# Performance work log

Hardware: AMD Instinct MI355X
Metric: run time of the kernel (lower is better)

Reference implementation:

```python
import jax, jax.numpy as jnp
import numpy as np

C = 1024
MID = C // 4  # 256
B, H, W = 16, 56, 56


def setup_inputs() -> dict:
    key = jax.random.key(0)
    ks = jax.random.split(key, 8)
    x = jax.random.normal(ks[0], (B, C, H, W), dtype=jnp.float32)
    gate_values = jax.random.uniform(ks[1], (B, MID), dtype=jnp.float32)
    # MoELayer conv weights: stack of out_channels 1x1 convs -> [out, in]
    W1 = jax.random.normal(ks[2], (MID, C), dtype=jnp.float32) * (1.0 / np.sqrt(C))
    b1 = jnp.zeros((MID,), dtype=jnp.float32)
    W2 = jax.random.normal(ks[3], (MID, MID), dtype=jnp.float32) * (1.0 / np.sqrt(MID))
    b2 = jnp.zeros((MID,), dtype=jnp.float32)
    W3 = jax.random.normal(ks[4], (C, MID), dtype=jnp.float32) * (1.0 / np.sqrt(MID))
    b3 = jnp.zeros((C,), dtype=jnp.float32)
    return {"x": x, "gate_values": gate_values, "W1": W1, "b1": b1,
            "W2": W2, "b2": b2, "W3": W3, "b3": b3}


def _moe_1x1(h, gate, Wc, bc):
    # Dense equivalent of the per-channel gated 1x1 conv experts:
    # out[b,o] = (conv_o(h[b]) ) * gate[b,o] if gate[b,o] > 0 else 0
    y = jnp.einsum('bchw,oc->bohw', h, Wc) + bc[None, :, None, None]
    g = jnp.where(gate > 0, gate, 0.0)  # [B, O]
    return y * g[:, :, None, None]


def reference(x, gate_values, W1, b1, W2, b2, W3, b3):
    h = jax.nn.relu(_moe_1x1(x, gate_values, W1, b1))
    h = jax.nn.relu(_moe_1x1(h, gate_values, W2, b2))
    h = jax.nn.relu(jnp.einsum('bchw,oc->bohw', h, W3) + b3[None, :, None, None])
    return h + x
```

## Files before the change

### kernel.cpp

```cpp
#include <hip/hip_runtime.h>


#define NPIX 3136
#define BATCH 16

typedef __attribute__((ext_vector_type(8))) short short8;
typedef __attribute__((ext_vector_type(4))) float v4f;

__device__ __forceinline__ unsigned short f2bf(float f) {
    union { float f; unsigned u; } v; v.f = f;
    unsigned r = v.u + 0x7fffu + ((v.u >> 16) & 1u);
    return (unsigned short)(r >> 16);
}

__device__ __forceinline__ void ld_g2l16(const unsigned short* g, unsigned short* l) {
    __builtin_amdgcn_global_load_lds(
        (const __attribute__((address_space(1))) unsigned int*)g,
        (__attribute__((address_space(3))) unsigned int*)l,
        16, 0, 0);
}

__global__ void convert_w(const float* __restrict__ W1, const float* __restrict__ W2,
                          const float* __restrict__ W3, unsigned short* __restrict__ Wb) {
    size_t e = ((size_t)blockIdx.x * 256 + threadIdx.x) * 4;
    const float* src; size_t off;
    if (e < 262144)      { src = W1; off = e; }
    else if (e < 327680) { src = W2; off = e - 262144; }
    else                 { src = W3; off = e - 327680; }
    float4 v = *reinterpret_cast<const float4*>(&src[off]);
    uint2 p;
    p.x = (unsigned)f2bf(v.x) | ((unsigned)f2bf(v.y) << 16);
    p.y = (unsigned)f2bf(v.z) | ((unsigned)f2bf(v.w) << 16);
    *reinterpret_cast<uint2*>(&Wb[e]) = p;
}

__global__ __launch_bounds__(256, 3) void moe_block(
    const float* __restrict__ x, const unsigned short* __restrict__ Wb,
    const float* __restrict__ b1, const float* __restrict__ b2,
    const float* __restrict__ b3, const float* __restrict__ gate,
    float* __restrict__ out)
{
    __shared__ __attribute__((aligned(16))) unsigned short Wsm[256 * 32];
    __shared__ __attribute__((aligned(16))) unsigned short Hsm[64 * 256];
    __shared__ __attribute__((aligned(16))) unsigned short Xsm[64 * 32];

    const unsigned short* W1b = Wb;
    const unsigned short* W2b = Wb + 262144;
    const unsigned short* W3b = Wb + 327680;

    const int b    = blockIdx.z;
    const int p0   = blockIdx.x * 64;
    const int t    = threadIdx.x;
    const int lane = t & 63;
    const int wave = t >> 6;
    const int wm   = wave * 64;
    const int l15  = lane & 15;
    const int quad = lane >> 4;

    const int srow  = t >> 2;
    const int skoff = (t & 3) * 8;

    char* hb = reinterpret_cast<char*>(Hsm);
    v4f acc[4][4];

    #pragma unroll
    for (int i = 0; i < 4; ++i)
        #pragma unroll
        for (int j = 0; j < 4; ++j) acc[i][j] = (v4f){0.f, 0.f, 0.f, 0.f};

    {
        const unsigned short* wg = W1b + srow * 1024 + skoff;
        const int cp   = t & 15;
        const int pgrp = t >> 4;
        const float* xg = x + ((size_t)(b * 1024 + 2 * cp)) * NPIX + p0 + pgrp * 4;
        unsigned* xw = reinterpret_cast<unsigned*>(&Xsm[pgrp * 128 + 2 * cp]);

        float4 a0 = *reinterpret_cast<const float4*>(xg);
        float4 a1 = *reinterpret_cast<const float4*>(xg + NPIX);

        for (int k0 = 0; k0 < 1024; k0 += 32) {
            __syncthreads();
            ld_g2l16(wg + k0,          &Wsm[t * 8]);
            ld_g2l16(wg + k0 + 65536,  &Wsm[2048 + t * 8]);
            ld_g2l16(wg + k0 + 131072, &Wsm[4096 + t * 8]);
            ld_g2l16(wg + k0 + 196608, &Wsm[6144 + t * 8]);
            unsigned u0 = (unsigned)f2bf(a0.x) | ((unsigned)f2bf(a1.x) << 16);
            unsigned u1 = (unsigned)f2bf(a0.y) | ((unsigned)f2bf(a1.y) << 16);
            unsigned u2 = (unsigned)f2bf(a0.z) | ((unsigned)f2bf(a1.z) << 16);
            unsigned u3 = (unsigned)f2bf(a0.w) | ((unsigned)f2bf(a1.w) << 16);
            xw[0] = u0; xw[16] = u1; xw[32] = u2; xw[48] = u3;
            __syncthreads();

            if (k0 + 32 < 1024) {
                const float* xp = xg + (size_t)(k0 + 32) * NPIX;
                a0 = *reinterpret_cast<const float4*>(xp);
                a1 = *reinterpret_cast<const float4*>(xp + NPIX);
            }

            short8 rf[4], cf[4];
            #pragma unroll
            for (int mt = 0; mt < 4; ++mt)
                rf[mt] = *reinterpret_cast<const short8*>(
                    &Wsm[(wm + mt * 16 + l15) * 32 + quad * 8]);
            #pragma unroll
            for (int nt = 0; nt < 4; ++nt)
                cf[nt] = *reinterpret_cast<const short8*>(
                    &Xsm[(nt * 16 + l15) * 32 + quad * 8]);
            #pragma unroll
            for (int mt = 0; mt < 4; ++mt)
                #pragma unroll
                for (int nt = 0; nt < 4; ++nt)
                    acc[mt][nt] = __builtin_amdgcn_mfma_f32_16x16x32_bf16(
                        rf[mt], cf[nt], acc[mt][nt], 0, 0, 0);
        }
    }

    #pragma unroll
    for (int mt = 0; mt < 4; ++mt) {
        const int o = wm + mt * 16 + quad * 4;
        const float4 bi = *reinterpret_cast<const float4*>(&b1[o]);
        const float4 gv = *reinterpret_cast<const float4*>(&gate[b * 256 + o]);
        const float g0 = gv.x > 0.f ? gv.x : 0.f;
        const float g1 = gv.y > 0.f ? gv.y : 0.f;
        const float g2 = gv.z > 0.f ? gv.z : 0.f;
        const float g3 = gv.w > 0.f ? gv.w : 0.f;
        #pragma unroll
        for (int nt = 0; nt < 4; ++nt) {
            const int pix = nt * 16 + l15;
            float v0 = (acc[mt][nt][0] + bi.x) * g0;
            float v1 = (acc[mt][nt][1] + bi.y) * g1;
            float v2 = (acc[mt][nt][2] + bi.z) * g2;
            float v3 = (acc[mt][nt][3] + bi.w) * g3;
            v0 = v0 > 0.f ? v0 : 0.f; v1 = v1 > 0.f ? v1 : 0.f;
            v2 = v2 > 0.f ? v2 : 0.f; v3 = v3 > 0.f ? v3 : 0.f;
            uint2 pq;
            pq.x = (unsigned)f2bf(v0) | ((unsigned)f2bf(v1) << 16);
            pq.y = (unsigned)f2bf(v2) | ((unsigned)f2bf(v3) << 16);
            const unsigned off = (unsigned)(pix * 512 + o * 2) ^ (unsigned)((pix & 7) << 4);
            *reinterpret_cast<uint2*>(hb + off) = pq;
        }
    }

    #pragma unroll
    for (int i = 0; i < 4; ++i)
        #pragma unroll
        for (int j = 0; j < 4; ++j) acc[i][j] = (v4f){0.f, 0.f, 0.f, 0.f};

    {
        const unsigned short* wg = W2b + srow * 256 + skoff;
        for (int k0 = 0; k0 < 256; k0 += 32) {
            __syncthreads();
            ld_g2l16(wg + k0,         &Wsm[t * 8]);
            ld_g2l16(wg + k0 + 16384, &Wsm[2048 + t * 8]);
            ld_g2l16(wg + k0 + 32768, &Wsm[4096 + t * 8]);
            ld_g2l16(wg + k0 + 49152, &Wsm[6144 + t * 8]);
            __syncthreads();

            short8 rf[4], cf[4];
            #pragma unroll
            for (int mt = 0; mt < 4; ++mt)
                rf[mt] = *reinterpret_cast<const short8*>(
                    &Wsm[(wm + mt * 16 + l15) * 32 + quad * 8]);
            #pragma unroll
            for (int nt = 0; nt < 4; ++nt) {
                const int row = nt * 16 + l15;
                const unsigned off =
                    (unsigned)(row * 512 + k0 * 2 + quad * 16) ^ (unsigned)((row & 7) << 4);
                cf[nt] = *reinterpret_cast<const short8*>(hb + off);
            }
            #pragma unroll
            for (int mt = 0; mt < 4; ++mt)
                #pragma unroll
                for (int nt = 0; nt < 4; ++nt)
                    acc[mt][nt] = __builtin_amdgcn_mfma_f32_16x16x32_bf16(
                        rf[mt], cf[nt], acc[mt][nt], 0, 0, 0);
        }
    }

    __syncthreads();

    #pragma unroll
    for (int mt = 0; mt < 4; ++mt) {
        const int o = wm + mt * 16 + quad * 4;
        const float4 bi = *reinterpret_cast<const float4*>(&b2[o]);
        const float4 gv = *reinterpret_cast<const float4*>(&gate[b * 256 + o]);
        const float g0 = gv.x > 0.f ? gv.x : 0.f;
        const float g1 = gv.y > 0.f ? gv.y : 0.f;
        const float g2 = gv.z > 0.f ? gv.z : 0.f;
        const float g3 = gv.w > 0.f ? gv.w : 0.f;
        #pragma unroll
        for (int nt = 0; nt < 4; ++nt) {
            const int pix = nt * 16 + l15;
            float v0 = (acc[mt][nt][0] + bi.x) * g0;
            float v1 = (acc[mt][nt][1] + bi.y) * g1;
            float v2 = (acc[mt][nt][2] + bi.z) * g2;
            float v3 = (acc[mt][nt][3] + bi.w) * g3;
            v0 = v0 > 0.f ? v0 : 0.f; v1 = v1 > 0.f ? v1 : 0.f;
            v2 = v2 > 0.f ? v2 : 0.f; v3 = v3 > 0.f ? v3 : 0.f;
            uint2 pq;
            pq.x = (unsigned)f2bf(v0) | ((unsigned)f2bf(v1) << 16);
            pq.y = (unsigned)f2bf(v2) | ((unsigned)f2bf(v3) << 16);
            const unsigned off = (unsigned)(pix * 512 + o * 2) ^ (unsigned)((pix & 7) << 4);
            *reinterpret_cast<uint2*>(hb + off) = pq;
        }
    }

    for (int ch = 0; ch < 4; ++ch) {
        const int oc0 = ch * 256;
        const unsigned short* wg = W3b + (size_t)(oc0 + srow) * 256 + skoff;

        #pragma unroll
        for (int i = 0; i < 4; ++i)
            #pragma unroll
            for (int j = 0; j < 4; ++j) acc[i][j] = (v4f){0.f, 0.f, 0.f, 0.f};

        for (int k0 = 0; k0 < 256; k0 += 32) {
            __syncthreads();
            ld_g2l16(wg + k0,         &Wsm[t * 8]);
            ld_g2l16(wg + k0 + 16384, &Wsm[2048 + t * 8]);
            ld_g2l16(wg + k0 + 32768, &Wsm[4096 + t * 8]);
            ld_g2l16(wg + k0 + 49152, &Wsm[6144 + t * 8]);
            __syncthreads();

            short8 rf[4], cf[4];
            #pragma unroll
            for (int mt = 0; mt < 4; ++mt) {
                const int row = mt * 16 + l15;
                const unsigned off =
                    (unsigned)(row * 512 + k0 * 2 + quad * 16) ^ (unsigned)((row & 7) << 4);
                rf[mt] = *reinterpret_cast<const short8*>(hb + off);
            }
            #pragma unroll
            for (int nt = 0; nt < 4; ++nt)
                cf[nt] = *reinterpret_cast<const short8*>(
                    &Wsm[(wm + nt * 16 + l15) * 32 + quad * 8]);
            #pragma unroll
            for (int mt = 0; mt < 4; ++mt)
                #pragma unroll
                for (int nt = 0; nt < 4; ++nt)
                    acc[mt][nt] = __builtin_amdgcn_mfma_f32_16x16x32_bf16(
                        rf[mt], cf[nt], acc[mt][nt], 0, 0, 0);
        }

        #pragma unroll
        for (int nt = 0; nt < 4; ++nt) {
            const int o = oc0 + wm + nt * 16 + l15;
            const float bi = b3[o];
            #pragma unroll
            for (int mt = 0; mt < 4; ++mt) {
                const int pix = p0 + mt * 16 + quad * 4;
                const size_t base = ((size_t)(b * 1024 + o)) * NPIX + pix;
                const float4 xr = *reinterpret_cast<const float4*>(&x[base]);
                float v0 = acc[mt][nt][0] + bi, v1 = acc[mt][nt][1] + bi;
                float v2 = acc[mt][nt][2] + bi, v3 = acc[mt][nt][3] + bi;
                float4 ov;
                ov.x = (v0 > 0.f ? v0 : 0.f) + xr.x;
                ov.y = (v1 > 0.f ? v1 : 0.f) + xr.y;
                ov.z = (v2 > 0.f ? v2 : 0.f) + xr.z;
                ov.w = (v3 > 0.f ? v3 : 0.f) + xr.w;
                *reinterpret_cast<float4*>(&out[base]) = ov;
            }
        }
    }
}

extern "C" void kernel_launch(void* const* d_in, const int* in_sizes, int n_in,
                              void* d_out, int out_size, void* d_ws, size_t ws_size,
                              hipStream_t stream) {
    const float* x    = (const float*)d_in[0];
    const float* gate = (const float*)d_in[1];
    const float* W1   = (const float*)d_in[2];
    const float* b1   = (const float*)d_in[3];
    const float* W2   = (const float*)d_in[4];
    const float* b2   = (const float*)d_in[5];
    const float* W3   = (const float*)d_in[6];
    const float* b3   = (const float*)d_in[7];
    float* out = (float*)d_out;

    unsigned short* Wb = (unsigned short*)d_ws;

    dim3 blk(256);
    convert_w<<<576, blk, 0, stream>>>(W1, W2, W3, Wb);
    moe_block<<<dim3(49, 1, BATCH), blk, 0, stream>>>(x, Wb, b1, b2, b3, gate, out);
}
```

Measured before the change: 494.9 us.

## Double-buffer weight tiles in LDS across all three GEMM stages

Doubles the weight LDS buffer and prefetches the next 32-wide weight tile (including across stage boundaries W1→W2→W3) while MFMAs consume the current one, cutting one barrier per iteration. The third stage is flattened into a single 32-step loop with an epilogue every 8 steps. LDS use rises, so launch bounds drop from 3 to 2 blocks per CU, trading occupancy for overlap of global-to-LDS loads with compute. The phase-1 barrier waits only on lgkmcnt for the LDS-bound loads, which relies on how global_load_lds completion is tracked.

```diff
diff --git a/kernel.cpp b/kernel.cpp
--- a/kernel.cpp
+++ b/kernel.cpp
@@ -18,6 +18,20 @@
         (const __attribute__((address_space(1))) unsigned int*)g,
         (__attribute__((address_space(3))) unsigned int*)l,
         16, 0, 0);
+}
+
+__device__ __forceinline__ void stage_w(const unsigned short* wg, int rowstride,
+                                        unsigned short* wr, int t) {
+    ld_g2l16(wg,                  wr + t * 8);
+    ld_g2l16(wg + 64 * rowstride, wr + 2048 + t * 8);
+    ld_g2l16(wg + 128 * rowstride, wr + 4096 + t * 8);
+    ld_g2l16(wg + 192 * rowstride, wr + 6144 + t * 8);
+}
+
+__device__ __forceinline__ void bar_lds_only() {
+    asm volatile("s_waitcnt lgkmcnt(0)" ::: "memory");
+    __builtin_amdgcn_s_barrier();
+    __builtin_amdgcn_sched_barrier(0);
 }
 
 __global__ void convert_w(const float* __restrict__ W1, const float* __restrict__ W2,
@@ -34,13 +48,13 @@
     *reinterpret_cast<uint2*>(&Wb[e]) = p;
 }
 
-__global__ __launch_bounds__(256, 3) void moe_block(
+__global__ __launch_bounds__(256, 2) void moe_block(
     const float* __restrict__ x, const unsigned short* __restrict__ Wb,
     const float* __restrict__ b1, const float* __restrict__ b2,
     const float* __restrict__ b3, const float* __restrict__ gate,
     float* __restrict__ out)
 {
-    __shared__ __attribute__((aligned(16))) unsigned short Wsm[256 * 32];
+    __shared__ __attribute__((aligned(16))) unsigned short Wsm[2 * 8192];
     __shared__ __attribute__((aligned(16))) unsigned short Hsm[64 * 256];
     __shared__ __attribute__((aligned(16))) unsigned short Xsm[64 * 32];
 
@@ -63,45 +77,51 @@
     char* hb = reinterpret_cast<char*>(Hsm);
     v4f acc[4][4];
 
+    const unsigned short* wg1 = W1b + srow * 1024 + skoff;
+    const unsigned short* wg2 = W2b + srow * 256 + skoff;
+    const unsigned short* wg3 = W3b + srow * 256 + skoff;
+
     #pragma unroll
     for (int i = 0; i < 4; ++i)
         #pragma unroll
         for (int j = 0; j < 4; ++j) acc[i][j] = (v4f){0.f, 0.f, 0.f, 0.f};
 
     {
-        const unsigned short* wg = W1b + srow * 1024 + skoff;
         const int cp   = t & 15;
         const int pgrp = t >> 4;
         const float* xg = x + ((size_t)(b * 1024 + 2 * cp)) * NPIX + p0 + pgrp * 4;
         unsigned* xw = reinterpret_cast<unsigned*>(&Xsm[pgrp * 128 + 2 * cp]);
 
+        stage_w(wg1, 1024, Wsm, t);
         float4 a0 = *reinterpret_cast<const float4*>(xg);
         float4 a1 = *reinterpret_cast<const float4*>(xg + NPIX);
-
-        for (int k0 = 0; k0 < 1024; k0 += 32) {
-            __syncthreads();
-            ld_g2l16(wg + k0,          &Wsm[t * 8]);
-            ld_g2l16(wg + k0 + 65536,  &Wsm[2048 + t * 8]);
-            ld_g2l16(wg + k0 + 131072, &Wsm[4096 + t * 8]);
-            ld_g2l16(wg + k0 + 196608, &Wsm[6144 + t * 8]);
+        __syncthreads();
+
+        for (int kt = 0; kt < 32; ++kt) {
+            unsigned short* rd = Wsm + (kt & 1) * 8192;
+            unsigned short* wr = Wsm + ((kt & 1) ^ 1) * 8192;
+
             unsigned u0 = (unsigned)f2bf(a0.x) | ((unsigned)f2bf(a1.x) << 16);
             unsigned u1 = (unsigned)f2bf(a0.y) | ((unsigned)f2bf(a1.y) << 16);
             unsigned u2 = (unsigned)f2bf(a0.z) | ((unsigned)f2bf(a1.z) << 16);
             unsigned u3 = (unsigned)f2bf(a0.w) | ((unsigned)f2bf(a1.w) << 16);
             xw[0] = u0; xw[16] = u1; xw[32] = u2; xw[48] = u3;
-            __syncthreads();
-
-            if (k0 + 32 < 1024) {
-                const float* xp = xg + (size_t)(k0 + 32) * NPIX;
+
+            if (kt < 31) stage_w(wg1 + (kt + 1) * 32, 1024, wr, t);
+            else         stage_w(wg2, 256, wr, t);
+            if (kt < 31) {
+                const float* xp = xg + (size_t)(kt + 1) * 32 * NPIX;
                 a0 = *reinterpret_cast<const float4*>(xp);
                 a1 = *reinterpret_cast<const float4*>(xp + NPIX);
             }
 
+            bar_lds_only();
+
             short8 rf[4], cf[4];
             #pragma unroll
             for (int mt = 0; mt < 4; ++mt)
                 rf[mt] = *reinterpret_cast<const short8*>(
-                    &Wsm[(wm + mt * 16 + l15) * 32 + quad * 8]);
+                    &rd[(wm + mt * 16 + l15) * 32 + quad * 8]);
             #pragma unroll
             for (int nt = 0; nt < 4; ++nt)
                 cf[nt] = *reinterpret_cast<const short8*>(
@@ -112,6 +132,8 @@
                 for (int nt = 0; nt < 4; ++nt)
                     acc[mt][nt] = __builtin_amdgcn_mfma_f32_16x16x32_bf16(
                         rf[mt], cf[nt], acc[mt][nt], 0, 0, 0);
+
+            __syncthreads();
         }
     }
 
@@ -140,44 +162,41 @@
             *reinterpret_cast<uint2*>(hb + off) = pq;
         }
     }
+    __syncthreads();
 
     #pragma unroll
     for (int i = 0; i < 4; ++i)
         #pragma unroll
         for (int j = 0; j < 4; ++j) acc[i][j] = (v4f){0.f, 0.f, 0.f, 0.f};
 
-    {
-        const unsigned short* wg = W2b + srow * 256 + skoff;
-        for (int k0 = 0; k0 < 256; k0 += 32) {
-            __syncthreads();
-            ld_g2l16(wg + k0,         &Wsm[t * 8]);
-            ld_g2l16(wg + k0 + 16384, &Wsm[2048 + t * 8]);
-            ld_g2l16(wg + k0 + 32768, &Wsm[4096 + t * 8]);
-            ld_g2l16(wg + k0 + 49152, &Wsm[6144 + t * 8]);
-            __syncthreads();
-
-            short8 rf[4], cf[4];
-            #pragma unroll
-            for (int mt = 0; mt < 4; ++mt)
-                rf[mt] = *reinterpret_cast<const short8*>(
-                    &Wsm[(wm + mt * 16 + l15) * 32 + quad * 8]);
-            #pragma unroll
-            for (int nt = 0; nt < 4; ++nt) {
-                const int row = nt * 16 + l15;
-                const unsigned off =
-                    (unsigned)(row * 512 + k0 * 2 + quad * 16) ^ (unsigned)((row & 7) << 4);
-                cf[nt] = *reinterpret_cast<const short8*>(hb + off);
-            }
-            #pragma unroll
-            for (int mt = 0; mt < 4; ++mt)
-                #pragma unroll
-                for (int nt = 0; nt < 4; ++nt)
-                    acc[mt][nt] = __builtin_amdgcn_mfma_f32_16x16x32_bf16(
-                        rf[mt], cf[nt], acc[mt][nt], 0, 0, 0);
-        }
-    }
-
-    __syncthreads();
+    for (int bt = 0; bt < 8; ++bt) {
+        unsigned short* rd = Wsm + (bt & 1) * 8192;
+        unsigned short* wr = Wsm + ((bt & 1) ^ 1) * 8192;
+        if (bt < 7) stage_w(wg2 + (bt + 1) * 32, 256, wr, t);
+        else        stage_w(wg3, 256, wr, t);
+
+        const int k0 = bt * 32;
+        short8 rf[4], cf[4];
+        #pragma unroll
+        for (int mt = 0; mt < 4; ++mt)
+            rf[mt] = *reinterpret_cast<const short8*>(
+                &rd[(wm + mt * 16 + l15) * 32 + quad * 8]);
+        #pragma unroll
+        for (int nt = 0; nt < 4; ++nt) {
+            const int row = nt * 16 + l15;
+            const unsigned off =
+                (unsigned)(row * 512 + k0 * 2 + quad * 16) ^ (unsigned)((row & 7) << 4);
+            cf[nt] = *reinterpret_cast<const short8*>(hb + off);
+        }
+        #pragma unroll
+        for (int mt = 0; mt < 4; ++mt)
+            #pragma unroll
+            for (int nt = 0; nt < 4; ++nt)
+                acc[mt][nt] = __builtin_amdgcn_mfma_f32_16x16x32_bf16(
+                    rf[mt], cf[nt], acc[mt][nt], 0, 0, 0);
+
+        __syncthreads();
+    }
 
     #pragma unroll
     for (int mt = 0; mt < 4; ++mt) {
@@ -204,62 +223,68 @@
             *reinterpret_cast<uint2*>(hb + off) = pq;
         }
     }
-
-    for (int ch = 0; ch < 4; ++ch) {
-        const int oc0 = ch * 256;
-        const unsigned short* wg = W3b + (size_t)(oc0 + srow) * 256 + skoff;
-
-        #pragma unroll
-        for (int i = 0; i < 4; ++i)
-            #pragma unroll
-            for (int j = 0; j < 4; ++j) acc[i][j] = (v4f){0.f, 0.f, 0.f, 0.f};
-
-        for (int k0 = 0; k0 < 256; k0 += 32) {
-            __syncthreads();
-            ld_g2l16(wg + k0,         &Wsm[t * 8]);
-            ld_g2l16(wg + k0 + 16384, &Wsm[2048 + t * 8]);
-            ld_g2l16(wg + k0 + 32768, &Wsm[4096 + t * 8]);
-            ld_g2l16(wg + k0 + 49152, &Wsm[6144 + t * 8]);
-            __syncthreads();
-
-            short8 rf[4], cf[4];
-            #pragma unroll
-            for (int mt = 0; mt < 4; ++mt) {
-                const int row = mt * 16 + l15;
-                const unsigned off =
-                    (unsigned)(row * 512 + k0 * 2 + quad * 16) ^ (unsigned)((row & 7) << 4);
-                rf[mt] = *reinterpret_cast<const short8*>(hb + off);
+    __syncthreads();
+
+    #pragma unroll
+    for (int i = 0; i < 4; ++i)
+        #pragma unroll
+        for (int j = 0; j < 4; ++j) acc[i][j] = (v4f){0.f, 0.f, 0.f, 0.f};
+
+    for (int jt = 0; jt < 32; ++jt) {
+        unsigned short* rd = Wsm + (jt & 1) * 8192;
+        unsigned short* wr = Wsm + ((jt & 1) ^ 1) * 8192;
+        if (jt < 31) {
+            const int jn = jt + 1;
+            stage_w(wg3 + (jn >> 3) * 65536 + (jn & 7) * 32, 256, wr, t);
+        }
+
+        const int k0 = (jt & 7) * 32;
+        short8 rf[4], cf[4];
+        #pragma unroll
+        for (int mt = 0; mt < 4; ++mt) {
+            const int row = mt * 16 + l15;
+            const unsigned off =
+                (unsigned)(row * 512 + k0 * 2 + quad * 16) ^ (unsigned)((row & 7) << 4);
+            rf[mt] = *reinterpret_cast<const short8*>(hb + off);
+        }
+        #pragma unroll
+        for (int nt = 0; nt < 4; ++nt)
+            cf[nt] = *reinterpret_cast<const short8*>(
+                &rd[(wm + nt * 16 + l15) * 32 + quad * 8]);
+        #pragma unroll
+        for (int mt = 0; mt < 4; ++mt)
+            #pragma unroll
+            for (int nt = 0; nt < 4; ++nt)
+                acc[mt][nt] = __builtin_amdgcn_mfma_f32_16x16x32_bf16(
+                    rf[mt], cf[nt], acc[mt][nt], 0, 0, 0);
+
+        __syncthreads();
+
+        if ((jt & 7) == 7) {
+            const int oc0 = (jt >> 3) * 256;
+            #pragma unroll
+            for (int nt = 0; nt < 4; ++nt) {
+                const int o = oc0 + wm + nt * 16 + l15;
+                const float bi = b3[o];
+                #pragma unroll
+                for (int mt = 0; mt < 4; ++mt) {
+                    const int pix = p0 + mt * 16 + quad * 4;
+                    const size_t base = ((size_t)(b * 1024 + o)) * NPIX + pix;
+                    const float4 xr = *reinterpret_cast<const float4*>(&x[base]);
+                    float v0 = acc[mt][nt][0] + bi, v1 = acc[mt][nt][1] + bi;
+                    float v2 = acc[mt][nt][2] + bi, v3 = acc[mt][nt][3] + bi;
+                    float4 ov;
+                    ov.x = (v0 > 0.f ? v0 : 0.f) + xr.x;
+                    ov.y = (v1 > 0.f ? v1 : 0.f) + xr.y;
+                    ov.z = (v2 > 0.f ? v2 : 0.f) + xr.z;
+                    ov.w = (v3 > 0.f ? v3 : 0.f) + xr.w;
+                    *reinterpret_cast<float4*>(&out[base]) = ov;
+                }
             }
             #pragma unroll
-            for (int nt = 0; nt < 4; ++nt)
-                cf[nt] = *reinterpret_cast<const short8*>(
-                    &Wsm[(wm + nt * 16 + l15) * 32 + quad * 8]);
-            #pragma unroll
-            for (int mt = 0; mt < 4; ++mt)
+            for (int i = 0; i < 4; ++i)
                 #pragma unroll
-                for (int nt = 0; nt < 4; ++nt)
-                    acc[mt][nt] = __builtin_amdgcn_mfma_f32_16x16x32_bf16(
-                        rf[mt], cf[nt], acc[mt][nt], 0, 0, 0);
-        }
-
-        #pragma unroll
-        for (int nt = 0; nt < 4; ++nt) {
-            const int o = oc0 + wm + nt * 16 + l15;
-            const float bi = b3[o];
-            #pragma unroll
-            for (int mt = 0; mt < 4; ++mt) {
-                const int pix = p0 + mt * 16 + quad * 4;
-                const size_t base = ((size_t)(b * 1024 + o)) * NPIX + pix;
-                const float4 xr = *reinterpret_cast<const float4*>(&x[base]);
-                float v0 = acc[mt][nt][0] + bi, v1 = acc[mt][nt][1] + bi;
-                float v2 = acc[mt][nt][2] + bi, v3 = acc[mt][nt][3] + bi;
-                float4 ov;
-                ov.x = (v0 > 0.f ? v0 : 0.f) + xr.x;
-                ov.y = (v1 > 0.f ? v1 : 0.f) + xr.y;
-                ov.z = (v2 > 0.f ? v2 : 0.f) + xr.z;
-                ov.w = (v3 > 0.f ? v3 : 0.f) + xr.w;
-                *reinterpret_cast<float4*>(&out[base]) = ov;
-            }
+                for (int j = 0; j < 4; ++j) acc[i][j] = (v4f){0.f, 0.f, 0.f, 0.f};
         }
     }
 }
```

New measurement: 502.8 us. About the same (+1.6%).
